# Optimization experiments

Hardware: AMD Instinct MI355X
Metric: run time of the kernel (lower is better)

The kernel has to match this reference:

```python
import jax, jax.numpy as jnp
import numpy as np

# G graphs of K atoms each, fully connected within graph (no self loops)
G, K, L, H, F, EMB, HID = 256, 16, 3, 3, 64, 200, 256
N = G * K
E = G * K * (K - 1)


def _wap(x, index, weights, num_seg, pw, gW1, gb1, gW2, gb2, mW1, mb1, mW2, mb2):
    """Roost WeightedAttentionPooling: segment softmax of gate_nn(x), scaled by
    weights**pow, applied to message_nn(x), segment-summed."""
    gate = jax.nn.selu(x @ gW1 + gb1) @ gW2 + gb2                      # [M]
    gmax = jax.ops.segment_max(gate, index, num_segments=num_seg)      # [S]
    gate = jnp.power(weights, pw) * jnp.exp(gate - gmax[index])        # [M]
    den = jax.ops.segment_sum(gate, index, num_segments=num_seg) + 1e-10
    attn = gate / den[index]                                           # [M]
    msg = jax.nn.selu(x @ mW1 + mb1) @ mW2 + mb2                       # [M,F]
    return jax.ops.segment_sum(attn[:, None] * msg, index, num_segments=num_seg)


def _wap_heads(x, index, weights, num_seg, params):
    f = lambda pw, gW1, gb1, gW2, gb2, mW1, mb1, mW2, mb2: _wap(
        x, index, weights, num_seg, pw, gW1, gb1, gW2, gb2, mW1, mb1, mW2, mb2)
    return jax.vmap(f)(*params)                                        # [H,S,F]


def setup_inputs() -> dict:
    key = jax.random.key(0)
    ks = jax.random.split(key, 16)
    # graph structure
    batch = jnp.repeat(jnp.arange(G, dtype=jnp.int32), K)              # [N]
    i = np.arange(K)
    src, dst = np.meshgrid(i, i, indexing="ij")
    mask = src != dst
    src, dst = src[mask], dst[mask]                                    # [K*(K-1)]
    offs = (np.arange(G) * K)[:, None]
    self_idx = jnp.asarray((offs + src[None, :]).reshape(-1), jnp.int32)
    nbr_idx = jnp.asarray((offs + dst[None, :]).reshape(-1), jnp.int32)

    s = lambda k, shape, fan_in: jax.random.normal(k, shape, jnp.float32) * (1.0 / fan_in) ** 0.5
    return dict(
        elem_weights=jax.random.uniform(ks[0], (N,), jnp.float32, 0.01, 1.0),
        elem_fea_in=jax.random.normal(ks[1], (N, EMB), jnp.float32),
        W_init=s(ks[2], (EMB, F - 1), EMB),
        b_init=jnp.zeros((F - 1,), jnp.float32),
        mg_W1=s(ks[3], (L, H, 2 * F, HID), 2 * F),
        mg_b1=jnp.zeros((L, H, HID), jnp.float32),
        mg_W2=s(ks[4], (L, H, HID), HID),
        mg_b2=jnp.zeros((L, H), jnp.float32),
        mm_W1=s(ks[5], (L, H, 2 * F, HID), 2 * F),
        mm_b1=jnp.zeros((L, H, HID), jnp.float32),
        mm_W2=s(ks[6], (L, H, HID, F), HID),
        mm_b2=jnp.zeros((L, H, F), jnp.float32),
        m_pow=jax.random.normal(ks[7], (L, H), jnp.float32),
        cg_W1=s(ks[8], (H, F, HID), F),
        cg_b1=jnp.zeros((H, HID), jnp.float32),
        cg_W2=s(ks[9], (H, HID), HID),
        cg_b2=jnp.zeros((H,), jnp.float32),
        cm_W1=s(ks[10], (H, F, HID), F),
        cm_b1=jnp.zeros((H, HID), jnp.float32),
        cm_W2=s(ks[11], (H, HID, F), HID),
        cm_b2=jnp.zeros((H, F), jnp.float32),
        c_pow=jax.random.normal(ks[12], (H,), jnp.float32),
        batch=batch,
        self_idx=self_idx,
        nbr_idx=nbr_idx,
    )


def reference(elem_weights, elem_fea_in, W_init, b_init,
              mg_W1, mg_b1, mg_W2, mg_b2, mm_W1, mm_b1, mm_W2, mm_b2, m_pow,
              cg_W1, cg_b1, cg_W2, cg_b2, cm_W1, cm_b1, cm_W2, cm_b2, c_pow,
              batch, self_idx, nbr_idx):
    w = elem_weights                                                   # [N]
    # initial embed: Linear(EMB, F-1) then concat fractional weight
    fea = jnp.concatenate([elem_fea_in @ W_init + b_init, w[:, None]], -1)  # [N,F]
    wn = w[nbr_idx]                                                    # [E]
    for l in range(L):
        pair = jnp.concatenate([fea[self_idx], fea[nbr_idx]], -1)      # [E,2F]
        heads = _wap_heads(pair, self_idx, wn, N,
                           (m_pow[l], mg_W1[l], mg_b1[l], mg_W2[l], mg_b2[l],
                            mm_W1[l], mm_b1[l], mm_W2[l], mm_b2[l]))   # [H,N,F]
        fea = fea + heads.mean(0)                                      # residual
    cry = _wap_heads(fea, batch, w, G,
                     (c_pow, cg_W1, cg_b1, cg_W2, cg_b2,
                      cm_W1, cm_b1, cm_W2, cm_b2))                     # [H,G,F]
    return cry.mean(0)                                                 # [G,F]
```

## Files before the change

### kernel.cpp

```cpp
#include <hip/hip_runtime.h>
#include <hip/hip_bf16.h>

#define G_ 256
#define K_ 16
#define L_ 3
#define H_ 3
#define F_ 64
#define EMB_ 200
#define HID_ 256
#define N_ (G_*K_)

typedef __attribute__((ext_vector_type(8))) short short8;
typedef __attribute__((ext_vector_type(4))) float f32x4;

#define SELU_S 1.0507009873554804934193349852946f
#define SELU_SA (1.0507009873554804934193349852946f*1.6732632423543772848170429916717f)
#define LOG2E_ 1.4426950408889634073599246810019f
#define SLN2_ (SELU_S*0.69314718055994530941723212145818f)

__device__ __forceinline__ float exp2_fast(float x) {
#if __has_builtin(__builtin_amdgcn_exp2f)
  return __builtin_amdgcn_exp2f(x);
#else
  return __exp2f(x);
#endif
}

__device__ __forceinline__ float selu_t(float t) {
  float tn = fminf(t, 0.f), tp = fmaxf(t, 0.f);
  return fmaf(SELU_SA, exp2_fast(tn), fmaf(SLN2_, tp, -SELU_SA));
}

__device__ __forceinline__ float selu_f(float x) {
  float e = __expf(x);
  float neg = fmaf(SELU_SA, e, -SELU_SA);
  float pos = SELU_S * x;
  return x > 0.f ? pos : neg;
}

__device__ __forceinline__ unsigned short f2bf(float x) {
  __hip_bfloat16 h = __float2bfloat16(x);
  return *reinterpret_cast<unsigned short*>(&h);
}

__device__ __forceinline__ unsigned int f2bf2(float a, float b) {
  float2 t; t.x = a; t.y = b;
  __hip_bfloat162 h = __float22bfloat162_rn(t);
  return *reinterpret_cast<unsigned int*>(&h);
}

__device__ __forceinline__ float bf2f(unsigned short u) {
  union { unsigned int i; float f; } v;
  v.i = ((unsigned int)u) << 16;
  return v.f;
}

__global__ __launch_bounds__(64) void init_embed(
    const float* __restrict__ fea_in, const float* __restrict__ W,
    const float* __restrict__ b, const float* __restrict__ wts,
    float* __restrict__ fea) {
  __shared__ float row[EMB_];
  int n = blockIdx.x;
  int j = threadIdx.x;
  for (int k = j; k < EMB_; k += 64) row[k] = fea_in[(size_t)n*EMB_ + k];
  __syncthreads();
  if (j < F_-1) {
    float s = b[j];
    for (int k = 0; k < EMB_; ++k) s = fmaf(row[k], W[k*(F_-1) + j], s);
    fea[(size_t)n*F_ + j] = s;
  } else {
    fea[(size_t)n*F_ + (F_-1)] = wts[n];
  }
}

__global__ __launch_bounds__(256) void prep_all(
    const float* __restrict__ mg_W1, const float* __restrict__ mm_W1,
    const float* __restrict__ mm_W2, const float* __restrict__ cg_W1,
    const float* __restrict__ cm_W1, const float* __restrict__ cm_W2,
    const float* __restrict__ mg_b1, const float* __restrict__ mm_b1,
    const float* __restrict__ cg_b1, const float* __restrict__ cm_b1,
    unsigned short* __restrict__ WcatT, unsigned short* __restrict__ W2mT,
    unsigned short* __restrict__ WcryT, unsigned short* __restrict__ W2cT,
    float* __restrict__ bias_e, float* __restrict__ bias_c,
    float* __restrict__ out0, float* __restrict__ feaZ) {
  int gt = blockIdx.x*256 + threadIdx.x, GT = gridDim.x*256;
  for (int idx = gt; idx < 9*1024*64; idx += GT) {
    int lh = idx >> 16, n = (idx >> 6) & 1023, k = idx & 63;
    const float* W = (n < 512) ? mg_W1 : mm_W1;
    int nn = n & 511;
    int r = (nn < 256) ? k : (64 + k);
    WcatT[idx] = f2bf(W[(size_t)lh*(2*F_*HID_) + r*HID_ + (nn & 255)]);
  }
  for (int idx = gt; idx < 9*64*256; idx += GT) {
    int lh = idx >> 14, f = (idx >> 8) & 63, k = idx & 255;
    W2mT[idx] = f2bf(mm_W2[(size_t)lh*(HID_*F_) + k*F_ + f]);
  }
  for (int idx = gt; idx < 1536*64; idx += GT) {
    int n = idx >> 6, k = idx & 63;
    int hh = n >> 9, r = n & 511;
    float v = (r < 256) ? cg_W1[(size_t)hh*F_*HID_ + k*HID_ + r]
                        : cm_W1[(size_t)hh*F_*HID_ + k*HID_ + (r - 256)];
    WcryT[idx] = f2bf(v);
  }
  for (int idx = gt; idx < 3*64*256; idx += GT) {
    int hh = idx >> 14, f = (idx >> 8) & 63, k = idx & 255;
    W2cT[idx] = f2bf(cm_W2[(size_t)hh*HID_*F_ + k*F_ + f]);
  }
  for (int idx = gt; idx < 9216 + 1536 + G_*F_; idx += GT) {
    if (idx < 9216) {
      int l = idx / 3072, c = idx - l*3072;
      int hh = c >> 10, cc = c & 1023;
      int lh = l*H_ + hh;
      float v = 0.f;
      if (cc < 256) v = mg_b1[lh*HID_ + cc];
      else if (cc >= 512 && cc < 768) v = mm_b1[lh*HID_ + (cc - 512)];
      bias_e[idx] = v;
    } else if (idx < 9216 + 1536) {
      int c = idx - 9216;
      int hh = c >> 9, cc = c & 511;
      bias_c[c] = (cc < 256) ? cg_b1[hh*HID_ + cc] : cm_b1[hh*HID_ + (cc - 256)];
    } else {
      out0[idx - 9216 - 1536] = 0.f;
    }
  }
  float4 z4; z4.x = 0.f; z4.y = 0.f; z4.z = 0.f; z4.w = 0.f;
  for (int idx = gt; idx < (3*N_*F_)/4; idx += GT)
    ((float4*)feaZ)[idx] = z4;
}

__global__ __launch_bounds__(512, 4) void edge_fused(
    const float* __restrict__ fea, const unsigned short* __restrict__ WcatT,
    const float* __restrict__ bias_e, const unsigned short* __restrict__ W2T,
    const float* __restrict__ mg_W2, const float* __restrict__ mg_b2,
    const float* __restrict__ m_pow, const float* __restrict__ mm_b2,
    const float* __restrict__ wts, float* __restrict__ fea_nxt, int l) {
  __shared__ __align__(16) unsigned short feaS[16][72];
  __shared__ __align__(16) unsigned short PQs[16][520];
  __shared__ __align__(16) unsigned short HbarS[16][264];
  __shared__ float bs[512];
  __shared__ float w2g[256];
  __shared__ float gred[240][2];
  __shared__ float gateA[240];
  __shared__ float sumat[16];
  __shared__ float wp[16];
  int t = threadIdx.x;
  int g = blockIdx.x, g16 = g * 16;
  int h = blockIdx.y, lh = l*H_ + h;
  const unsigned short* Wlh = WcatT + (size_t)lh*1024*64;
  const float* biaslh = bias_e + (size_t)l*3072 + h*1024;
  int w = t >> 6, lane = t & 63, mr = lane & 15, q = lane >> 4;

  {
    int row = t >> 5, c2 = (t & 31) * 2;
    float2 fv = *(const float2*)&fea[(size_t)(g16 + row)*64 + c2];
    *(unsigned int*)&feaS[row][c2] = f2bf2(fv.x, fv.y);
  }
  bs[t] = biaslh[t];
  if (t < 256) w2g[t] = mg_W2[lh*HID_ + t];
  __syncthreads();

  {
    int n0w = w * 64;
    short8 a0 = *(const short8*)&feaS[mr][q*8];
    short8 a1 = *(const short8*)&feaS[mr][32 + q*8];
    #pragma unroll
    for (int nt = 0; nt < 4; ++nt) {
      int n = n0w + nt*16 + mr;
      const unsigned short* bp = Wlh + (size_t)n*64 + q*8;
      short8 b0 = *(const short8*)bp;
      short8 b1 = *(const short8*)(bp + 32);
      f32x4 z = {0.f, 0.f, 0.f, 0.f};
      z = __builtin_amdgcn_mfma_f32_16x16x32_bf16(a0, b0, z, 0, 0, 0);
      z = __builtin_amdgcn_mfma_f32_16x16x32_bf16(a1, b1, z, 0, 0, 0);
      float bb = bs[n];
      #pragma unroll
      for (int r = 0; r < 4; ++r)
        PQs[q*4 + r][n] = f2bf((z[r] + bb) * LOG2E_);
    }
  }
  __syncthreads();

  {
    float nb = biaslh[512 + t];
    if (t < 480) {
      int e = t >> 1, half = t & 1;
      int i = e / 15, jj = e - i*15;
      int j = (jj < i) ? jj : jj + 1;
      float s = 0.f;
      #pragma unroll
      for (int u = 0; u < 16; ++u) {
        int c = half*8 + u*16;
        short8 pv = *(const short8*)&PQs[i][c];
        short8 qv = *(const short8*)&PQs[j][256 + c];
        #pragma unroll
        for (int r = 0; r < 8; ++r) {
          float hv = selu_t(bf2f((unsigned short)pv[r]) + bf2f((unsigned short)qv[r]));
          s = fmaf(hv, w2g[c + r], s);
        }
      }
      gred[e][half] = s;
    } else if (t < 496) {
      wp[t - 480] = __powf(wts[g16 + (t - 480)], m_pow[lh]);
    }
    bs[t] = nb;
  }
  __syncthreads();

  {
    int n0w = w * 64;
    short8 a0 = *(const short8*)&feaS[mr][q*8];
    short8 a1 = *(const short8*)&feaS[mr][32 + q*8];
    #pragma unroll
    for (int nt = 0; nt < 4; ++nt) {
      int n = n0w + nt*16 + mr;
      const unsigned short* bp = Wlh + (size_t)(512 + n)*64 + q*8;
      short8 b0 = *(const short8*)bp;
      short8 b1 = *(const short8*)(bp + 32);
      f32x4 z = {0.f, 0.f, 0.f, 0.f};
      z = __builtin_amdgcn_mfma_f32_16x16x32_bf16(a0, b0, z, 0, 0, 0);
      z = __builtin_amdgcn_mfma_f32_16x16x32_bf16(a1, b1, z, 0, 0, 0);
      float bb = bs[n];
      #pragma unroll
      for (int r = 0; r < 4; ++r)
        PQs[q*4 + r][n] = f2bf((z[r] + bb) * LOG2E_);
    }
  }
  if (t < 16) {
    int i = t;
    float b2v = mg_b2[lh];
    float gl[15];
    float m = -1e30f;
    #pragma unroll
    for (int jj = 0; jj < 15; ++jj) {
      float v = gred[i*15 + jj][0] + gred[i*15 + jj][1] + b2v;
      gl[jj] = v; m = fmaxf(m, v);
    }
    float den = 0.f;
    #pragma unroll
    for (int jj = 0; jj < 15; ++jj) {
      int j = (jj < i) ? jj : jj + 1;
      float x = wp[j] * __expf(gl[jj] - m);
      gl[jj] = x; den += x;
    }
    den += 1e-10f;
    float sa = 0.f;
    #pragma unroll
    for (int jj = 0; jj < 15; ++jj) {
      float a = gl[jj] / den; gateA[i*15 + jj] = a; sa += a;
    }
    sumat[i] = sa;
  }
  __syncthreads();

  {
    int i = t >> 5, k0 = (t & 31) * 8;
    short8 pv = *(const short8*)&PQs[i][k0];
    float pf[8];
    #pragma unroll
    for (int r = 0; r < 8; ++r) pf[r] = bf2f((unsigned short)pv[r]);
    float hb[8] = {0.f, 0.f, 0.f, 0.f, 0.f, 0.f, 0.f, 0.f};
    for (int jj = 0; jj < 15; ++jj) {
      int j = (jj < i) ? jj : jj + 1;
      float a = gateA[i*15 + jj];
      short8 qv = *(const short8*)&PQs[j][256 + k0];
      #pragma unroll
      for (int r = 0; r < 8; ++r) {
        float hv = selu_t(pf[r] + bf2f((unsigned short)qv[r]));
        hb[r] = fmaf(a, hv, hb[r]);
      }
    }
    unsigned int hpk[4];
    #pragma unroll
    for (int r2 = 0; r2 < 4; ++r2) hpk[r2] = f2bf2(hb[2*r2], hb[2*r2+1]);
    *(short8*)&HbarS[i][k0] = *reinterpret_cast<short8*>(hpk);
  }
  __syncthreads();

  if (w < 4) {
    const unsigned short* W2lh = W2T + (size_t)lh*64*256;
    f32x4 acc = {0.f, 0.f, 0.f, 0.f};
    #pragma unroll
    for (int kc = 0; kc < 8; ++kc) {
      short8 a = *(const short8*)&HbarS[mr][kc*32 + q*8];
      short8 b = *(const short8*)&W2lh[(size_t)(w*16 + mr)*256 + kc*32 + q*8];
      acc = __builtin_amdgcn_mfma_f32_16x16x32_bf16(a, b, acc, 0, 0, 0);
    }
    int f = w*16 + mr;
    float b2 = mm_b2[lh*F_ + f];
    #pragma unroll
    for (int r = 0; r < 4; ++r) {
      int i = q*4 + r;
      float val = (acc[r] + b2*sumat[i]) * (1.f/3.f);
      if (h == 0) val += fea[(size_t)(g16 + i)*64 + f];
      atomicAdd(&fea_nxt[(size_t)(g16 + i)*64 + f], val);
    }
  }
}

__global__ __launch_bounds__(256) void cry_fused(
    const float* __restrict__ fea, const unsigned short* __restrict__ WcryT,
    const float* __restrict__ bias_c, const unsigned short* __restrict__ W2cT,
    const float* __restrict__ cg_W2, const float* __restrict__ cg_b2,
    const float* __restrict__ cm_b2, const float* __restrict__ c_pow,
    const float* __restrict__ wts, float* __restrict__ out) {
  __shared__ __align__(16) unsigned short feaS[16][72];
  __shared__ float PQh[16][520];
  __shared__ float bsc[512];
  __shared__ float gred[16][18];
  __shared__ float attnL[16];
  __shared__ float sumatS;
  __shared__ __align__(16) unsigned short hidc[16][264];
  int t = threadIdx.x;
  int g = blockIdx.x, g16 = g*16, h = blockIdx.y;
  {
    int row = t >> 4, c4 = (t & 15) * 4;
    float4 fv = *(const float4*)&fea[(size_t)(g16 + row)*64 + c4];
    *(unsigned int*)&feaS[row][c4]   = f2bf2(fv.x, fv.y);
    *(unsigned int*)&feaS[row][c4+2] = f2bf2(fv.z, fv.w);
  }
  bsc[t] = bias_c[h*512 + t];
  bsc[256 + t] = bias_c[h*512 + 256 + t];
  int w = t >> 6, lane = t & 63, mr = lane & 15, q = lane >> 4;
  __syncthreads();
  {
    int n0w = w * 128;
    short8 a0 = *(const short8*)&feaS[mr][q*8];
    short8 a1 = *(const short8*)&feaS[mr][32 + q*8];
    #pragma unroll
    for (int nt = 0; nt < 8; ++nt) {
      int n = n0w + nt*16 + mr;
      const unsigned short* bp = WcryT + (size_t)(h*512 + n)*64 + q*8;
      short8 b0 = *(const short8*)bp;
      short8 b1 = *(const short8*)(bp + 32);
      f32x4 z = {0.f, 0.f, 0.f, 0.f};
      z = __builtin_amdgcn_mfma_f32_16x16x32_bf16(a0, b0, z, 0, 0, 0);
      z = __builtin_amdgcn_mfma_f32_16x16x32_bf16(a1, b1, z, 0, 0, 0);
      float bb = bsc[n];
      #pragma unroll
      for (int r = 0; r < 4; ++r)
        PQh[q*4 + r][n] = (z[r] + bb) * LOG2E_;
    }
  }
  __syncthreads();
  {
    int i = t >> 4, c0 = (t & 15) * 16;
    float s = 0.f;
    #pragma unroll
    for (int c = c0; c < c0+16; ++c)
      s = fmaf(selu_t(PQh[i][c]), cg_W2[h*HID_ + c], s);
    gred[i][t & 15] = s;
  }
  __syncthreads();
  if (t < 16) {
    float sg = 0.f;
    #pragma unroll
    for (int u2 = 0; u2 < 16; ++u2) sg += gred[t][u2];
    gred[t][16] = sg + cg_b2[h];
  }
  __syncthreads();
  if (t == 0) {
    float pw = c_pow[h];
    float m = -1e30f;
    #pragma unroll
    for (int i = 0; i < 16; ++i) m = fmaxf(m, gred[i][16]);
    float den = 0.f; float v[16];
    #pragma unroll
    for (int i = 0; i < 16; ++i) {
      float x = __powf(wts[g16+i], pw) * __expf(gred[i][16] - m);
      v[i] = x; den += x;
    }
    den += 1e-10f;
    float sa = 0.f;
    #pragma unroll
    for (int i = 0; i < 16; ++i) { float a = v[i]/den; attnL[i] = a; sa += a; }
    sumatS = sa;
  }
  {
    int i = t >> 4, c0 = (t & 15) * 16;
    #pragma unroll
    for (int c = c0; c < c0+16; c += 2) {
      unsigned int pk = f2bf2(selu_t(PQh[i][256 + c]), selu_t(PQh[i][256 + c + 1]));
      *(unsigned int*)&hidc[i][c] = pk;
    }
  }
  __syncthreads();
  f32x4 acc = {0.f, 0.f, 0.f, 0.f};
  #pragma unroll
  for (int kc = 0; kc < 8; ++kc) {
    short8 a = *(const short8*)&hidc[mr][kc*32 + q*8];
    short8 b = *(const short8*)&W2cT[((size_t)h*64 + w*16 + mr)*HID_ + kc*32 + q*8];
    acc = __builtin_amdgcn_mfma_f32_16x16x32_bf16(a, b, acc, 0, 0, 0);
  }
  float p = 0.f;
  #pragma unroll
  for (int r = 0; r < 4; ++r) p = fmaf(attnL[q*4+r], acc[r], p);
  p += __shfl_xor(p, 16);
  p += __shfl_xor(p, 32);
  if (q == 0) {
    int f = w*16 + mr;
    atomicAdd(&out[(size_t)g*64 + f],
              (p + cm_b2[h*F_ + f]*sumatS) * (1.f/(float)H_));
  }
}

extern "C" void kernel_launch(void* const* d_in, const int* in_sizes, int n_in,
                              void* d_out, int out_size, void* d_ws, size_t ws_size,
                              hipStream_t stream) {
  const float* elem_weights = (const float*)d_in[0];
  const float* elem_fea_in  = (const float*)d_in[1];
  const float* W_init = (const float*)d_in[2];
  const float* b_init = (const float*)d_in[3];
  const float* mg_W1  = (const float*)d_in[4];
  const float* mg_b1  = (const float*)d_in[5];
  const float* mg_W2  = (const float*)d_in[6];
  const float* mg_b2  = (const float*)d_in[7];
  const float* mm_W1  = (const float*)d_in[8];
  const float* mm_b1  = (const float*)d_in[9];
  const float* mm_W2  = (const float*)d_in[10];
  const float* mm_b2  = (const float*)d_in[11];
  const float* m_pow  = (const float*)d_in[12];
  const float* cg_W1  = (const float*)d_in[13];
  const float* cg_b1  = (const float*)d_in[14];
  const float* cg_W2  = (const float*)d_in[15];
  const float* cg_b2  = (const float*)d_in[16];
  const float* cm_W1  = (const float*)d_in[17];
  const float* cm_b1  = (const float*)d_in[18];
  const float* cm_W2  = (const float*)d_in[19];
  const float* cm_b2  = (const float*)d_in[20];
  const float* c_pow  = (const float*)d_in[21];
  float* out = (float*)d_out;

  float* ws = (float*)d_ws;
  float* feaA  = ws;
  float* feaB  = feaA + (size_t)N_*F_;
  float* feaC  = feaB + (size_t)N_*F_;
  float* feaD  = feaC + (size_t)N_*F_;
  unsigned short* WcatT = (unsigned short*)(feaD + (size_t)N_*F_);
  unsigned short* W2mT  = WcatT + (size_t)9*1024*64;
  unsigned short* WcryT = W2mT  + (size_t)9*64*256;
  unsigned short* W2cT  = WcryT + (size_t)1536*64;
  float* bias_e = (float*)(W2cT + (size_t)3*64*256);
  float* bias_c = bias_e + 9216;

  prep_all<<<256, 256, 0, stream>>>(mg_W1, mm_W1, mm_W2, cg_W1, cm_W1, cm_W2,
                                    mg_b1, mm_b1, cg_b1, cm_b1,
                                    WcatT, W2mT, WcryT, W2cT, bias_e, bias_c,
                                    out, feaB);
  init_embed<<<N_, 64, 0, stream>>>(elem_fea_in, W_init, b_init, elem_weights, feaA);

  float* bufs[4] = {feaA, feaB, feaC, feaD};
  for (int l = 0; l < L_; ++l) {
    edge_fused<<<dim3(G_, H_), 512, 0, stream>>>(
        bufs[l], WcatT, bias_e, W2mT, mg_W2, mg_b2, m_pow, mm_b2,
        elem_weights, bufs[l+1], l);
  }

  cry_fused<<<dim3(G_, H_), 256, 0, stream>>>(
      bufs[3], WcryT, bias_c, W2cT, cg_W2, cg_b2, cm_b2, c_pow,
      elem_weights, out);
}
```

Before: 241.9 us.

## Merge init embed into weight prep kernel and drop log2e prescale

```diff
diff --git a/kernel.cpp b/kernel.cpp
--- a/kernel.cpp
+++ b/kernel.cpp
@@ -55,25 +55,7 @@
   return v.f;
 }
 
-__global__ __launch_bounds__(64) void init_embed(
-    const float* __restrict__ fea_in, const float* __restrict__ W,
-    const float* __restrict__ b, const float* __restrict__ wts,
-    float* __restrict__ fea) {
-  __shared__ float row[EMB_];
-  int n = blockIdx.x;
-  int j = threadIdx.x;
-  for (int k = j; k < EMB_; k += 64) row[k] = fea_in[(size_t)n*EMB_ + k];
-  __syncthreads();
-  if (j < F_-1) {
-    float s = b[j];
-    for (int k = 0; k < EMB_; ++k) s = fmaf(row[k], W[k*(F_-1) + j], s);
-    fea[(size_t)n*F_ + j] = s;
-  } else {
-    fea[(size_t)n*F_ + (F_-1)] = wts[n];
-  }
-}
-
-__global__ __launch_bounds__(256) void prep_all(
+__global__ __launch_bounds__(256) void prep_init_all(
     const float* __restrict__ mg_W1, const float* __restrict__ mm_W1,
     const float* __restrict__ mm_W2, const float* __restrict__ cg_W1,
     const float* __restrict__ cm_W1, const float* __restrict__ cm_W2,
@@ -82,8 +64,27 @@
     unsigned short* __restrict__ WcatT, unsigned short* __restrict__ W2mT,
     unsigned short* __restrict__ WcryT, unsigned short* __restrict__ W2cT,
     float* __restrict__ bias_e, float* __restrict__ bias_c,
-    float* __restrict__ out0, float* __restrict__ feaZ) {
-  int gt = blockIdx.x*256 + threadIdx.x, GT = gridDim.x*256;
+    float* __restrict__ out0, float* __restrict__ feaZ,
+    const float* __restrict__ fea_in, const float* __restrict__ W_init,
+    const float* __restrict__ b_init, const float* __restrict__ wts,
+    float* __restrict__ feaA) {
+  int bid = blockIdx.x, tid = threadIdx.x;
+  if (bid >= 256) {
+    __shared__ float row[4][EMB_];
+    int sub = tid >> 6, j = tid & 63;
+    int n = (bid - 256) * 4 + sub;
+    for (int k = j; k < EMB_; k += 64) row[sub][k] = fea_in[(size_t)n*EMB_ + k];
+    __syncthreads();
+    if (j < F_-1) {
+      float s = b_init[j];
+      for (int k = 0; k < EMB_; ++k) s = fmaf(row[sub][k], W_init[k*(F_-1) + j], s);
+      feaA[(size_t)n*F_ + j] = s;
+    } else {
+      feaA[(size_t)n*F_ + (F_-1)] = wts[n];
+    }
+    return;
+  }
+  int gt = bid*256 + tid, GT = 256*256;
   for (int idx = gt; idx < 9*1024*64; idx += GT) {
     int lh = idx >> 16, n = (idx >> 6) & 1023, k = idx & 63;
     const float* W = (n < 512) ? mg_W1 : mm_W1;
@@ -175,7 +176,7 @@
       float bb = bs[n];
       #pragma unroll
       for (int r = 0; r < 4; ++r)
-        PQs[q*4 + r][n] = f2bf((z[r] + bb) * LOG2E_);
+        PQs[q*4 + r][n] = f2bf(z[r] + bb);
     }
   }
   __syncthreads();
@@ -194,7 +195,7 @@
         short8 qv = *(const short8*)&PQs[j][256 + c];
         #pragma unroll
         for (int r = 0; r < 8; ++r) {
-          float hv = selu_t(bf2f((unsigned short)pv[r]) + bf2f((unsigned short)qv[r]));
+          float hv = selu_f(bf2f((unsigned short)pv[r]) + bf2f((unsigned short)qv[r]));
           s = fmaf(hv, w2g[c + r], s);
         }
       }
@@ -222,7 +223,7 @@
       float bb = bs[n];
       #pragma unroll
       for (int r = 0; r < 4; ++r)
-        PQs[q*4 + r][n] = f2bf((z[r] + bb) * LOG2E_);
+        PQs[q*4 + r][n] = f2bf(z[r] + bb);
     }
   }
   if (t < 16) {
@@ -265,7 +266,7 @@
       short8 qv = *(const short8*)&PQs[j][256 + k0];
       #pragma unroll
       for (int r = 0; r < 8; ++r) {
-        float hv = selu_t(pf[r] + bf2f((unsigned short)qv[r]));
+        float hv = selu_f(pf[r] + bf2f((unsigned short)qv[r]));
         hb[r] = fmaf(a, hv, hb[r]);
       }
     }
@@ -442,11 +443,12 @@
   float* bias_e = (float*)(W2cT + (size_t)3*64*256);
   float* bias_c = bias_e + 9216;
 
-  prep_all<<<256, 256, 0, stream>>>(mg_W1, mm_W1, mm_W2, cg_W1, cm_W1, cm_W2,
-                                    mg_b1, mm_b1, cg_b1, cm_b1,
-                                    WcatT, W2mT, WcryT, W2cT, bias_e, bias_c,
-                                    out, feaB);
-  init_embed<<<N_, 64, 0, stream>>>(elem_fea_in, W_init, b_init, elem_weights, feaA);
+  prep_init_all<<<256 + N_/4, 256, 0, stream>>>(
+      mg_W1, mm_W1, mm_W2, cg_W1, cm_W1, cm_W2,
+      mg_b1, mm_b1, cg_b1, cm_b1,
+      WcatT, W2mT, WcryT, W2cT, bias_e, bias_c,
+      out, feaB,
+      elem_fea_in, W_init, b_init, elem_weights, feaA);
 
   float* bufs[4] = {feaA, feaB, feaC, feaD};
   for (int l = 0; l < L_; ++l) {
```

Measured after the change: 235.7 us, median of 3. -2.6%, faster.
